# Optimization experiments

Hardware: AMD Instinct MI355X
Metric: run time of the kernel (lower is better)

The kernel has to match this reference:

```python
import jax, jax.numpy as jnp
import numpy as np

C = 80          # NUM_CLASSES
D = 8525        # total anchors over FPN levels (640 input: 80^2+40^2+20^2+10^2+5^2)
B = 64
EPS = 1e-6


def setup_inputs() -> dict:
    key = jax.random.key(0)
    ks = jax.random.split(key, 8)
    outs = jax.random.normal(ks[0], (B, D, C + 5), dtype=jnp.float32)
    grids = jax.random.uniform(ks[1], (D, 2), dtype=jnp.float32) * 640.0  # anchor centers (px)
    # --- build gres = [gcls(C), centerness(1), g_ltrb(4), mask_pp(1), mask_pos(1), pad(1)] ---
    labels = jax.random.randint(ks[2], (B, D), 0, C)
    mask_pos = (jax.random.uniform(ks[3], (B, D)) < 0.10).astype(jnp.float32)  # in-box positives
    mask_pp = (jax.random.uniform(ks[4], (B, D)) < 0.05).astype(jnp.float32)   # center-radius positives
    gcls = jax.nn.one_hot(labels, C, dtype=jnp.float32) * mask_pos[..., None]
    gcenterness = jax.random.uniform(ks[5], (B, D), dtype=jnp.float32)
    off = jax.random.uniform(ks[6], (B, D, 4), dtype=jnp.float32) * 64.0 + 1.0
    gx = grids[None, :, 0]
    gy = grids[None, :, 1]
    g_ltrb = jnp.stack([gx - off[..., 0], gy - off[..., 1],
                        gx + off[..., 2], gy + off[..., 3]], axis=-1)
    gres = jnp.concatenate([gcls,
                            gcenterness[..., None],
                            g_ltrb,
                            mask_pp[..., None],
                            mask_pos[..., None],
                            jnp.zeros((B, D, 1), jnp.float32)], axis=-1)  # [B, D, 88]
    nums_pos = jax.random.randint(ks[7], (B,), 1, 21).astype(jnp.int32)
    return {"outs": outs, "gres": gres, "grids": grids, "nums_pos": nums_pos}


def _giou(p, g):
    # elementwise GIoU on ltrb boxes, p/g: [..., 4]
    ix1 = jnp.maximum(p[..., 0], g[..., 0]); iy1 = jnp.maximum(p[..., 1], g[..., 1])
    ix2 = jnp.minimum(p[..., 2], g[..., 2]); iy2 = jnp.minimum(p[..., 3], g[..., 3])
    inter = jnp.clip(ix2 - ix1, 0.0) * jnp.clip(iy2 - iy1, 0.0)
    area_p = jnp.clip(p[..., 2] - p[..., 0], 0.0) * jnp.clip(p[..., 3] - p[..., 1], 0.0)
    area_g = jnp.clip(g[..., 2] - g[..., 0], 0.0) * jnp.clip(g[..., 3] - g[..., 1], 0.0)
    union = area_p + area_g - inter
    iou = inter / (union + EPS)
    cx1 = jnp.minimum(p[..., 0], g[..., 0]); cy1 = jnp.minimum(p[..., 1], g[..., 1])
    cx2 = jnp.maximum(p[..., 2], g[..., 2]); cy2 = jnp.maximum(p[..., 3], g[..., 3])
    c_area = (cx2 - cx1) * (cy2 - cy1)
    return iou - (c_area - union) / (c_area + EPS)


def reference(outs, gres, grids, nums_pos):
    np_f = nums_pos.astype(jnp.float32)
    # ---- cls: focal loss over all anchors ----
    pcls = jax.nn.sigmoid(outs[..., :C])          # [B, D, C]
    gcls = gres[..., :C]
    pos_m = (gcls == 1.0).astype(pcls.dtype)
    l_pos = -0.25 * (1.0 - pcls) ** 2 * jnp.log(pcls + EPS) * pos_m
    l_neg = -0.75 * pcls ** 2 * jnp.log(1.0 - pcls + EPS) * (1.0 - pos_m)
    l_cls_pos = jnp.mean(jnp.sum(l_pos, axis=(1, 2)) / np_f)
    l_cls_neg = jnp.mean(jnp.sum(l_neg, axis=(1, 2)) / np_f)
    # ---- conf: BCE(pconf, 1) over center-radius positives ----
    mask_pp = (gres[..., C + 5] == 1.0).astype(outs.dtype)
    pconf = jax.nn.sigmoid(outs[..., C])
    bce = -jnp.log(pconf + EPS)                    # target = ones
    l_conf = 5.0 * jnp.mean(jnp.sum(bce * mask_pp, axis=-1) / np_f)
    # ---- reg: masked GIoU over in-box positives ----
    mask_pos = (gres[..., C + 6] == 1.0).astype(outs.dtype)
    poff = outs[..., C + 1:C + 5]
    gxy = grids[None]                              # [1, D, 2]
    pboxes = jnp.concatenate([gxy - poff[..., :2], gxy + poff[..., 2:]], axis=-1)
    g_ltrb = gres[..., C + 1:C + 5]
    giou = _giou(pboxes, g_ltrb)                   # [B, D]
    gcenter = gres[..., C]
    n_pos = jnp.maximum(jnp.sum(mask_pos), 1.0)
    l_reg = 5.0 * jnp.sum((1.0 - giou) * gcenter * mask_pos) / n_pos
    return l_cls_pos + l_cls_neg + l_conf + l_reg
```

## Files before the change

### kernel.cpp

```cpp
#include <hip/hip_runtime.h>

namespace {

constexpr int   kC    = 80;
constexpr int   kD    = 8525;
constexpr int   kB    = 64;
constexpr float kEps  = 1e-6f;
constexpr int   kOC   = 85;
constexpr int   kGC   = 88;
constexpr int   kBlk  = 256;
constexpr int   kPB   = kD * kOC;

constexpr int   kRowPerB    = 6;
constexpr int   kNRow       = kB * kRowPerB;
constexpr int   kStreamPerB = 26;
constexpr int   kNStream    = kB * kStreamPerB;
constexpr int   kNT         = kNRow + kNStream;
constexpr int   kChunk = (kPB + kStreamPerB - 1) / kStreamPerB;
constexpr int   kRPB   = (kD + kRowPerB - 1) / kRowPerB;

constexpr int   kQCap = 320;
constexpr int   kQW   = 8;

__device__ __forceinline__ float wave_reduce(float v) {
#pragma unroll
  for (int o = 32; o > 0; o >>= 1) v += __shfl_down(v, o, 64);
  return v;
}

__device__ __forceinline__ float fast_rcp(float x) {
  return __builtin_amdgcn_rcpf(x);
}

__device__ __forceinline__ float lneg_raw(float x) {
  const float p = fast_rcp(1.0f + __expf(-x));
  return p * p * __logf(1.0f - p + kEps);
}

__device__ __forceinline__ float lneg4(const float4 v) {
  return (lneg_raw(v.x) + lneg_raw(v.y)) + (lneg_raw(v.z) + lneg_raw(v.w));
}

__global__ __launch_bounds__(kBlk, 8) void floss_fused(
    const float* __restrict__ outs, const float* __restrict__ gres,
    const float* __restrict__ grids, const int* __restrict__ nums_pos,
    float* __restrict__ partials) {
  const int bid = blockIdx.x;
  const int tid = threadIdx.x;

  __shared__ float s_q[kQCap * kQW];
  __shared__ int   s_cnt;
  __shared__ float sm[3][kBlk / 64];

  float pm = 0.f, pr = 0.f, pn = 0.f;

  if (bid >= kNRow) {
    const int sid = bid - kNRow;
    const int b   = sid / kStreamPerB;
    const int s   = sid - b * kStreamPerB;
    const float scale = fast_rcp(64.0f * (float)nums_pos[b]);
    const int e0 = s * kChunk;
    const int e1 = (e0 + kChunk < kPB) ? e0 + kChunk : kPB;
    const int gA = b * kPB + e0;
    const int gB = b * kPB + e1;
    const int gv = (gA + 3) & ~3;
    const int nvec = (gB - gv) >> 2;
    const int gvend = gv + (nvec << 2);
    float a0 = 0.f, a1 = 0.f, a2 = 0.f, a3 = 0.f;
    if (tid < gv - gA)    a0 += lneg_raw(outs[gA + tid]);
    if (tid < gB - gvend) a1 += lneg_raw(outs[gvend + tid]);
    const float* pv = outs + gv;
    int v = tid;
    for (; v + 3 * kBlk < nvec; v += 4 * kBlk) {
      const float4 xa = *(const float4*)(pv + 4 * v);
      const float4 xb = *(const float4*)(pv + 4 * (v + kBlk));
      const float4 xc = *(const float4*)(pv + 4 * (v + 2 * kBlk));
      const float4 xd = *(const float4*)(pv + 4 * (v + 3 * kBlk));
      a0 += lneg4(xa);
      a1 += lneg4(xb);
      a2 += lneg4(xc);
      a3 += lneg4(xd);
    }
    for (; v < nvec; v += kBlk) a0 += lneg4(*(const float4*)(pv + 4 * v));
    pm = -0.75f * scale * ((a0 + a1) + (a2 + a3));
  } else {
    const int b  = bid / kRowPerB;
    const int s  = bid - b * kRowPerB;
    const int r0 = s * kRPB;
    const int r1 = (r0 + kRPB < kD) ? r0 + kRPB : kD;
    const float scale = fast_rcp(64.0f * (float)nums_pos[b]);

    if (tid == 0) s_cnt = 0;
    __syncthreads();

    for (int r = r0 + tid; r < r1; r += kBlk) {
      const int row = b * kD + r;
      const float4 xt = *(const float4*)(outs + (size_t)row * kOC + 80);
      const float  x84 = outs[(size_t)row * kOC + 84];
      const float4 t1 = *(const float4*)(gres + (size_t)row * kGC + 84);
      const float t5 = ((lneg_raw(xt.x) + lneg_raw(xt.y)) +
                        (lneg_raw(xt.z) + lneg_raw(xt.w))) + lneg_raw(x84);
      pm += 0.75f * scale * t5;
      if (t1.y == 1.0f) {
        const float pc = fast_rcp(1.0f + __expf(-xt.x));
        pm += -5.0f * __logf(pc + kEps) * scale;
      }
      if (t1.z == 1.0f) {
        pn += 1.0f;
        const int slot = atomicAdd(&s_cnt, 1);
        if (slot < kQCap) {
          float* q = s_q + slot * kQW;
          q[0] = __int_as_float(row);
          q[1] = xt.y; q[2] = xt.z; q[3] = xt.w; q[4] = x84;
          q[5] = grids[2 * r + 0];
          q[6] = grids[2 * r + 1];
          q[7] = t1.x;
        }
      }
    }
    __syncthreads();

    const int nq = (s_cnt < kQCap) ? s_cnt : kQCap;
    const int hh = tid >> 5;
    const int h  = tid & 31;
    for (int e = hh; e < nq; e += 8) {
      const float* q = s_q + e * kQW;
      const int row = __float_as_int(q[0]);
      int cand = -1;
      float4 v = make_float4(0.f, 0.f, 0.f, 0.f);
      if (h < 20) {
        v = *(const float4*)(gres + (size_t)row * kGC + 4 * h);
        if (v.x == 1.0f) cand = 4 * h;
        if (v.y == 1.0f) cand = 4 * h + 1;
        if (v.z == 1.0f) cand = 4 * h + 2;
        if (v.w == 1.0f) cand = 4 * h + 3;
      } else if (h == 20) {
        v = *(const float4*)(gres + (size_t)row * kGC + 80);
      }
#pragma unroll
      for (int m = 16; m > 0; m >>= 1) {
        const int o = __shfl_xor(cand, m, 32);
        cand = (o > cand) ? o : cand;
      }
      if (h == 20 && cand >= 0) {
        const float x  = outs[(size_t)row * kOC + cand];
        const float p  = fast_rcp(1.0f + __expf(-x));
        const float om = 1.0f - p;
        const float lp = -0.25f * om * om * __logf(p + kEps);
        const float ln = -0.75f * p * p * __logf(om + kEps);
        pm += (lp - ln) * scale;
        const float gx = q[5], gy = q[6];
        const float p0 = gx - q[1], p1 = gy - q[2];
        const float p2 = gx + q[3], p3 = gy + q[4];
        const float g0 = v.y, g1 = v.z, g2 = v.w, g3 = q[7];
        const float iw = fmaxf(fminf(p2, g2) - fmaxf(p0, g0), 0.f);
        const float ih = fmaxf(fminf(p3, g3) - fmaxf(p1, g1), 0.f);
        const float inter = iw * ih;
        const float ap = fmaxf(p2 - p0, 0.f) * fmaxf(p3 - p1, 0.f);
        const float ag = fmaxf(g2 - g0, 0.f) * fmaxf(g3 - g1, 0.f);
        const float un = ap + ag - inter;
        const float iou = inter * fast_rcp(un + kEps);
        const float ca = (fmaxf(p2, g2) - fminf(p0, g0)) *
                         (fmaxf(p3, g3) - fminf(p1, g1));
        const float giou = iou - (ca - un) * fast_rcp(ca + kEps);
        pr += (1.0f - giou) * v.x;
      }
    }
  }

  const float vm = wave_reduce(pm);
  const float vr = wave_reduce(pr);
  const float vn = wave_reduce(pn);
  const int lane = tid & 63;
  const int w    = tid >> 6;
  if (lane == 0) { sm[0][w] = vm; sm[1][w] = vr; sm[2][w] = vn; }
  __syncthreads();
  if (tid == 0) {
    float m = 0.f, r = 0.f, n = 0.f;
#pragma unroll
    for (int j = 0; j < kBlk / 64; ++j) { m += sm[0][j]; r += sm[1][j]; n += sm[2][j]; }
    partials[bid * 3 + 0] = m;
    partials[bid * 3 + 1] = r;
    partials[bid * 3 + 2] = n;
  }
}

__global__ __launch_bounds__(kBlk) void floss_final(
    const float* __restrict__ partials, float* __restrict__ out) {
  float m = 0.f, r = 0.f, n = 0.f;
  for (int i = threadIdx.x; i < kNT; i += kBlk) {
    m += partials[i * 3 + 0];
    r += partials[i * 3 + 1];
    n += partials[i * 3 + 2];
  }
  __shared__ float sm[3][kBlk / 64];
  m = wave_reduce(m); r = wave_reduce(r); n = wave_reduce(n);
  const int lane = threadIdx.x & 63;
  const int w    = threadIdx.x >> 6;
  if (lane == 0) { sm[0][w] = m; sm[1][w] = r; sm[2][w] = n; }
  __syncthreads();
  if (threadIdx.x == 0) {
    float tm = 0.f, tr = 0.f, tn = 0.f;
#pragma unroll
    for (int j = 0; j < kBlk / 64; ++j) { tm += sm[0][j]; tr += sm[1][j]; tn += sm[2][j]; }
    out[0] = tm + 5.0f * tr / fmaxf(tn, 1.0f);
  }
}

}

extern "C" void kernel_launch(void* const* d_in, const int* in_sizes, int n_in,
                              void* d_out, int out_size, void* d_ws, size_t ws_size,
                              hipStream_t stream) {
  const float* outs     = (const float*)d_in[0];
  const float* gres     = (const float*)d_in[1];
  const float* grids    = (const float*)d_in[2];
  const int*   nums_pos = (const int*)d_in[3];
  float* partials = (float*)d_ws;

  floss_fused<<<kNT, kBlk, 0, stream>>>(outs, gres, grids, nums_pos, partials);
  floss_final<<<1, kBlk, 0, stream>>>(partials, (float*)d_out);
}
```

Before: 77.27 us.

## Unify stream and row blocks into per-slice blocks with alternating phase order

Replaces the split between dedicated streaming blocks and row-processing blocks with a uniform grid where each block handles one contiguous slice of anchors. Within that slice it does both the dense negative-loss streaming and the per-row conf/reg work, and the phase order alternates across blocks to mix memory- and compute-heavy phases. The sigmoid/log math switches to raw exp2/log2 intrinsics with the ln2 factor folded out, and the positive-queue capacity is shrunk. The aim is to balance load and cut transcendental cost. The risk is that a slice overflowing the smaller queue would silently drop positives.

```diff
diff --git a/kernel.cpp b/kernel.cpp
--- a/kernel.cpp
+++ b/kernel.cpp
@@ -10,17 +10,14 @@
 constexpr int   kGC   = 88;
 constexpr int   kBlk  = 256;
 constexpr int   kPB   = kD * kOC;
-
-constexpr int   kRowPerB    = 6;
-constexpr int   kNRow       = kB * kRowPerB;
-constexpr int   kStreamPerB = 26;
-constexpr int   kNStream    = kB * kStreamPerB;
-constexpr int   kNT         = kNRow + kNStream;
-constexpr int   kChunk = (kPB + kStreamPerB - 1) / kStreamPerB;
-constexpr int   kRPB   = (kD + kRowPerB - 1) / kRowPerB;
-
-constexpr int   kQCap = 320;
-constexpr int   kQW   = 8;
+constexpr int   kSpb  = 32;
+constexpr int   kRPS  = (kD + kSpb - 1) / kSpb;
+constexpr int   kNT   = kB * kSpb;
+constexpr int   kQCap = 96;
+constexpr int   kQW   = 9;
+
+constexpr float kLog2e = 1.44269504f;
+constexpr float kLn2   = 0.69314718f;
 
 __device__ __forceinline__ float wave_reduce(float v) {
 #pragma unroll
@@ -32,13 +29,14 @@
   return __builtin_amdgcn_rcpf(x);
 }
 
-__device__ __forceinline__ float lneg_raw(float x) {
-  const float p = fast_rcp(1.0f + __expf(-x));
-  return p * p * __logf(1.0f - p + kEps);
-}
-
-__device__ __forceinline__ float lneg4(const float4 v) {
-  return (lneg_raw(v.x) + lneg_raw(v.y)) + (lneg_raw(v.z) + lneg_raw(v.w));
+__device__ __forceinline__ float lneg2(float x) {
+  const float t = __builtin_amdgcn_exp2f(x * -kLog2e);
+  const float p = fast_rcp(1.0f + t);
+  return p * p * __builtin_amdgcn_logf(1.000001f - p);
+}
+
+__device__ __forceinline__ float lneg2_4(const float4 v) {
+  return (lneg2(v.x) + lneg2(v.y)) + (lneg2(v.z) + lneg2(v.w));
 }
 
 __global__ __launch_bounds__(kBlk, 8) void floss_fused(
@@ -47,79 +45,77 @@
     float* __restrict__ partials) {
   const int bid = blockIdx.x;
   const int tid = threadIdx.x;
+  const int b   = bid >> 5;
+  const int sb  = bid & 31;
+  const int r0  = sb * kRPS;
+  const int r1  = (r0 + kRPS < kD) ? r0 + kRPS : kD;
+  const int nrows = r1 - r0;
+  const float scale = fast_rcp(64.0f * (float)nums_pos[b]);
 
   __shared__ float s_q[kQCap * kQW];
   __shared__ int   s_cnt;
   __shared__ float sm[3][kBlk / 64];
-
-  float pm = 0.f, pr = 0.f, pn = 0.f;
-
-  if (bid >= kNRow) {
-    const int sid = bid - kNRow;
-    const int b   = sid / kStreamPerB;
-    const int s   = sid - b * kStreamPerB;
-    const float scale = fast_rcp(64.0f * (float)nums_pos[b]);
-    const int e0 = s * kChunk;
-    const int e1 = (e0 + kChunk < kPB) ? e0 + kChunk : kPB;
-    const int gA = b * kPB + e0;
-    const int gB = b * kPB + e1;
+  if (tid == 0) s_cnt = 0;
+
+  float accS = 0.f;
+  float accT = 0.f;
+  float pmO  = 0.f;
+  float pr = 0.f, pn = 0.f;
+
+  auto streamPhase = [&]() {
+    const int gA = b * kPB + r0 * kOC;
+    const int gB = b * kPB + r1 * kOC;
     const int gv = (gA + 3) & ~3;
     const int nvec = (gB - gv) >> 2;
     const int gvend = gv + (nvec << 2);
     float a0 = 0.f, a1 = 0.f, a2 = 0.f, a3 = 0.f;
-    if (tid < gv - gA)    a0 += lneg_raw(outs[gA + tid]);
-    if (tid < gB - gvend) a1 += lneg_raw(outs[gvend + tid]);
-    const float* pv = outs + gv;
+    if (tid < gv - gA)    a0 += lneg2(outs[gA + tid]);
+    if (tid < gB - gvend) a1 += lneg2(outs[gvend + tid]);
+    const float4* pv = (const float4*)(outs + gv);
     int v = tid;
     for (; v + 3 * kBlk < nvec; v += 4 * kBlk) {
-      const float4 xa = *(const float4*)(pv + 4 * v);
-      const float4 xb = *(const float4*)(pv + 4 * (v + kBlk));
-      const float4 xc = *(const float4*)(pv + 4 * (v + 2 * kBlk));
-      const float4 xd = *(const float4*)(pv + 4 * (v + 3 * kBlk));
-      a0 += lneg4(xa);
-      a1 += lneg4(xb);
-      a2 += lneg4(xc);
-      a3 += lneg4(xd);
+      const float4 xa = pv[v];
+      const float4 xb = pv[v + kBlk];
+      const float4 xc = pv[v + 2 * kBlk];
+      const float4 xd = pv[v + 3 * kBlk];
+      a0 += lneg2_4(xa);
+      a1 += lneg2_4(xb);
+      a2 += lneg2_4(xc);
+      a3 += lneg2_4(xd);
     }
-    for (; v < nvec; v += kBlk) a0 += lneg4(*(const float4*)(pv + 4 * v));
-    pm = -0.75f * scale * ((a0 + a1) + (a2 + a3));
-  } else {
-    const int b  = bid / kRowPerB;
-    const int s  = bid - b * kRowPerB;
-    const int r0 = s * kRPB;
-    const int r1 = (r0 + kRPB < kD) ? r0 + kRPB : kD;
-    const float scale = fast_rcp(64.0f * (float)nums_pos[b]);
-
-    if (tid == 0) s_cnt = 0;
-    __syncthreads();
-
-    for (int r = r0 + tid; r < r1; r += kBlk) {
+    for (; v < nvec; v += kBlk) a0 += lneg2_4(pv[v]);
+    accS += (a0 + a1) + (a2 + a3);
+  };
+
+  auto rowStage1 = [&]() {
+    for (int rl = tid; rl < nrows; rl += kBlk) {
+      const int r   = r0 + rl;
       const int row = b * kD + r;
-      const float4 xt = *(const float4*)(outs + (size_t)row * kOC + 80);
+      const float4 xt  = *(const float4*)(outs + (size_t)row * kOC + 80);
       const float  x84 = outs[(size_t)row * kOC + 84];
-      const float4 t1 = *(const float4*)(gres + (size_t)row * kGC + 84);
-      const float t5 = ((lneg_raw(xt.x) + lneg_raw(xt.y)) +
-                        (lneg_raw(xt.z) + lneg_raw(xt.w))) + lneg_raw(x84);
-      pm += 0.75f * scale * t5;
+      const float4 t1  = *(const float4*)(gres + (size_t)row * kGC + 84);
+      accT += ((lneg2(xt.x) + lneg2(xt.y)) +
+               (lneg2(xt.z) + lneg2(xt.w))) + lneg2(x84);
       if (t1.y == 1.0f) {
         const float pc = fast_rcp(1.0f + __expf(-xt.x));
-        pm += -5.0f * __logf(pc + kEps) * scale;
+        pmO += -5.0f * __logf(pc + kEps) * scale;
       }
       if (t1.z == 1.0f) {
         pn += 1.0f;
         const int slot = atomicAdd(&s_cnt, 1);
         if (slot < kQCap) {
           float* q = s_q + slot * kQW;
+          const float2 gxy = *(const float2*)(grids + 2 * r);
           q[0] = __int_as_float(row);
           q[1] = xt.y; q[2] = xt.z; q[3] = xt.w; q[4] = x84;
-          q[5] = grids[2 * r + 0];
-          q[6] = grids[2 * r + 1];
+          q[5] = gxy.x; q[6] = gxy.y;
           q[7] = t1.x;
         }
       }
     }
-    __syncthreads();
-
+  };
+
+  auto rowStage2 = [&]() {
     const int nq = (s_cnt < kQCap) ? s_cnt : kQCap;
     const int hh = tid >> 5;
     const int h  = tid & 31;
@@ -148,7 +144,7 @@
         const float om = 1.0f - p;
         const float lp = -0.25f * om * om * __logf(p + kEps);
         const float ln = -0.75f * p * p * __logf(om + kEps);
-        pm += (lp - ln) * scale;
+        pmO += (lp - ln) * scale;
         const float gx = q[5], gy = q[6];
         const float p0 = gx - q[1], p1 = gy - q[2];
         const float p2 = gx + q[3], p3 = gy + q[4];
@@ -166,7 +162,23 @@
         pr += (1.0f - giou) * v.x;
       }
     }
-  }
+  };
+
+  if (((bid >> 8) ^ bid) & 1) {
+    streamPhase();
+    __syncthreads();
+    rowStage1();
+    __syncthreads();
+    rowStage2();
+  } else {
+    __syncthreads();
+    rowStage1();
+    __syncthreads();
+    rowStage2();
+    streamPhase();
+  }
+
+  float pm = 0.75f * kLn2 * scale * (accT - accS) + pmO;
 
   const float vm = wave_reduce(pm);
   const float vr = wave_reduce(pr);
```

Measured after the change: 64.39 us. 1.2x faster.
